# Performance work log

Measured on AMD Instinct MI355X. Metric: run time of the kernel, lower is better.

Reference implementation:

```python
import jax, jax.numpy as jnp
import numpy as np

NUM_GRAPHS = 1024
NODES_PER_GRAPH = 116
DEG = 32
IN_CH = 116
HID = 32
EPS = 1e-5


def setup_inputs() -> dict:
    key = jax.random.key(0)
    ks = jax.random.split(key, 16)
    N = NUM_GRAPHS * NODES_PER_GRAPH
    E = N * DEG
    x = jax.random.normal(ks[0], (N, IN_CH), dtype=jnp.float32)
    # edges stay within each graph: graph id per edge, then random src/dst node in that graph
    gid = jnp.arange(E, dtype=jnp.int64) // (NODES_PER_GRAPH * DEG)
    off = gid * NODES_PER_GRAPH
    src = off + jax.random.randint(ks[1], (E,), 0, NODES_PER_GRAPH, dtype=jnp.int64)
    dst = off + jax.random.randint(ks[2], (E,), 0, NODES_PER_GRAPH, dtype=jnp.int64)
    edge_index = jnp.stack([src, dst], axis=0)
    edge_weight = jax.random.uniform(ks[3], (E,), dtype=jnp.float32)
    batch = jnp.arange(N, dtype=jnp.int64) // NODES_PER_GRAPH
    xavier = lambda k, fi, fo: jax.random.uniform(k, (fi, fo), jnp.float32, -1.0, 1.0) * np.sqrt(6.0 / (fi + fo))
    return {
        "x": x, "edge_index": edge_index, "edge_weight": edge_weight, "batch": batch,
        "W1": xavier(ks[4], IN_CH, HID), "b1": jnp.zeros((HID,), jnp.float32),
        "g1": jnp.ones((HID,), jnp.float32), "be1": jnp.zeros((HID,), jnp.float32),
        "W2": xavier(ks[5], HID, 2 * HID), "b2": jnp.zeros((2 * HID,), jnp.float32),
        "g2": jnp.ones((2 * HID,), jnp.float32), "be2": jnp.zeros((2 * HID,), jnp.float32),
        "Wf1": xavier(ks[6], 4 * HID, HID), "bf1": jnp.zeros((HID,), jnp.float32),
        "gf": jnp.ones((HID,), jnp.float32), "bef": jnp.zeros((HID,), jnp.float32),
        "Wf2": xavier(ks[7], HID, 2), "bf2": jnp.zeros((2,), jnp.float32),
    }


def _gcn_conv(x, row, col, ew, W, b):
    """PyG GCNConv: linear -> add self-loops -> sym-normalized scatter-add -> +bias."""
    N = x.shape[0]
    h = x @ W  # [N, out]
    loop = jnp.arange(N, dtype=row.dtype)
    row_sl = jnp.concatenate([row, loop])
    col_sl = jnp.concatenate([col, loop])
    w_sl = jnp.concatenate([ew, jnp.ones((N,), ew.dtype)])
    deg = jax.ops.segment_sum(w_sl, col_sl, num_segments=N)
    dinv = jnp.where(deg > 0, jax.lax.rsqrt(deg), 0.0)
    norm = dinv[row_sl] * w_sl * dinv[col_sl]  # [E+N]
    msg = h[row_sl] * norm[:, None]            # gather + scale
    out = jax.ops.segment_sum(msg, col_sl, num_segments=N)
    return out + b


def _bn(x, g, b):
    # BatchNorm1d in training mode: biased batch stats over axis 0
    m = jnp.mean(x, axis=0)
    v = jnp.mean(jnp.square(x - m), axis=0)
    return (x - m) * jax.lax.rsqrt(v + EPS) * g + b


def reference(x, edge_index, edge_weight, batch, W1, b1, g1, be1, W2, b2, g2, be2,
              Wf1, bf1, gf, bef, Wf2, bf2):
    row, col = edge_index[0], edge_index[1]
    h = jax.nn.relu(_bn(_gcn_conv(x, row, col, edge_weight, W1, b1), g1, be1))
    h = jax.nn.relu(_bn(_gcn_conv(h, row, col, edge_weight, W2, b2), g2, be2))
    # global mean / max pool over graphs
    counts = jax.ops.segment_sum(jnp.ones((h.shape[0],), h.dtype), batch, num_segments=NUM_GRAPHS)
    x_mean = jax.ops.segment_sum(h, batch, num_segments=NUM_GRAPHS) / counts[:, None]
    x_max = jax.ops.segment_max(h, batch, num_segments=NUM_GRAPHS)
    emb = jnp.concatenate([x_mean, x_max], axis=1)  # [G, 4*HID]
    z = jax.nn.relu(_bn(emb @ Wf1 + bf1, gf, bef))  # dropout = identity (eval)
    return z @ Wf2 + bf2  # [G, num_classes]
```

## Files before the change

### kernel.cpp

```cpp
#include <hip/hip_runtime.h>

#define NPG 116
#define EPG (NPG * 32)
#define HID 32
#define HID2 64
#define EPS 1e-5f

#define WFS 132
#define AS 136
#define YSS 40
#define HPG 7424

using bf16x8 = __attribute__((ext_vector_type(8))) short;
using f32x4  = __attribute__((ext_vector_type(4))) float;

__device__ __forceinline__ unsigned short f2bf(float f) {
  union { float f; unsigned int i; } cv;
  cv.f = f;
  unsigned int x = cv.i;
  x += 0x7fff + ((x >> 16) & 1);
  return (unsigned short)(x >> 16);
}
__device__ __forceinline__ float bf2f(unsigned int u) {
  union { unsigned int i; float f; } cv;
  cv.i = u << 16;
  return cv.f;
}

#define MFMA16(a, b, c) __builtin_amdgcn_mfma_f32_16x16x32_bf16((a), (b), (c), 0, 0, 0)


__global__ __launch_bounds__(256) void k_lin1(const float* __restrict__ x,
                                              const float* __restrict__ W1,
                                              float* __restrict__ h1reg,
                                              int N) {
  __shared__ __align__(16) short W1T[HID * AS];
  const int g = blockIdx.x, tid = threadIdx.x;
  const int nb = g * NPG;
  const int l = tid & 63, w = tid >> 6;
  const int rf = l & 15, kg = l >> 4;

  { int* p = (int*)W1T;
    for (int i = tid; i < HID * AS / 2; i += 256) p[i] = 0; }
  __syncthreads();
  for (int i = tid; i < NPG * HID; i += 256) {
    int k = i >> 5, c = i & 31;
    W1T[c * AS + k] = (short)f2bf(W1[i]);
  }
  __syncthreads();

  unsigned short* lb = (unsigned short*)(h1reg + (size_t)g * 3712);
  for (int t = w; t < 16; t += 4) {
    const int mt = t >> 1, nt = t & 1;
    const int rl = mt * 16 + rf;
    f32x4 acc = {0.f, 0.f, 0.f, 0.f};
#pragma unroll
    for (int kk = 0; kk < 4; ++kk) {
      bf16x8 a;
      if (rl < NPG) {
        const float* xr = x + (size_t)(nb + rl) * NPG;
        if (kk < 3) {
          const float4* xp = (const float4*)(xr + kk * 32 + kg * 8);
          float4 v0 = xp[0], v1 = xp[1];
          a[0] = (short)f2bf(v0.x); a[1] = (short)f2bf(v0.y);
          a[2] = (short)f2bf(v0.z); a[3] = (short)f2bf(v0.w);
          a[4] = (short)f2bf(v1.x); a[5] = (short)f2bf(v1.y);
          a[6] = (short)f2bf(v1.z); a[7] = (short)f2bf(v1.w);
        } else {
          const int k0 = 96 + kg * 8;
#pragma unroll
          for (int j = 0; j < 8; ++j) {
            int k = k0 + j;
            a[j] = (k < NPG) ? (short)f2bf(xr[k]) : (short)0;
          }
        }
      } else {
#pragma unroll
        for (int j = 0; j < 8; ++j) a[j] = 0;
      }
      bf16x8 b = *(const bf16x8*)&W1T[(nt * 16 + rf) * AS + kk * 32 + kg * 8];
      acc = MFMA16(a, b, acc);
    }
    const int col = nt * 16 + rf;
#pragma unroll
    for (int i = 0; i < 4; ++i) {
      int row = mt * 16 + kg * 4 + i;
      if (row < NPG) lb[row * HID + col] = f2bf(acc[i]);
    }
  }
}

__global__ __launch_bounds__(1024) void k_conv1(const int* __restrict__ ei,
                                                const float* __restrict__ ew,
                                                float* __restrict__ h1reg,
                                                float* __restrict__ dinvg,
                                                float* __restrict__ stats,
                                                float* __restrict__ buf,
                                                int N, int E) {
  __shared__ __align__(16) float Wf[NPG * WFS];
  __shared__ __align__(16) short L1T[HID * AS];
  __shared__ float degs[NPG];
  __shared__ float ss[HID], qs[HID];
  const int g = blockIdx.x, tid = threadIdx.x;
  const int nb = g * NPG, e0 = g * EPG;
  const int* rowp = ei;
  const int* colp = ei + E;
  const int l = tid & 63, w = tid >> 6;
  const int rf = l & 15, kg = l >> 4;

  for (int i = tid; i < NPG; i += 1024) degs[i] = 1.0f;
  if (tid < HID) { ss[tid] = 0.0f; qs[tid] = 0.0f; }
  { float4* p = (float4*)Wf;
    for (int i = tid; i < NPG * WFS / 4; i += 1024) p[i] = make_float4(0,0,0,0); }
  { int* p = (int*)L1T;
    for (int i = tid; i < HID * AS / 2; i += 1024) p[i] = 0; }
  __syncthreads();

  for (int e = tid; e < EPG; e += 1024) {
    int eg = e0 + e;
    int s = rowp[eg] - nb, d = colp[eg] - nb;
    float wv = ew[eg];
    atomicAdd(&degs[d], wv);
    atomicAdd(&Wf[d * WFS + s], wv);
  }
  if (tid < NPG) atomicAdd(&Wf[tid * WFS + tid], 1.0f);
  __syncthreads();

  if (tid < NPG) dinvg[nb + tid] = rsqrtf(degs[tid]);
  {
    const unsigned int* lb32 =
        (const unsigned int*)(h1reg + (size_t)g * 3712);
    for (int i = tid; i < NPG * 16; i += 1024) {
      int row = i >> 4, c2 = (i & 15) * 2;
      unsigned int u = lb32[i];
      float dr = rsqrtf(degs[row]);
      L1T[c2 * AS + row] = (short)f2bf(bf2f(u & 0xffffu) * dr);
      L1T[(c2 + 1) * AS + row] = (short)f2bf(bf2f(u >> 16) * dr);
    }
    int* wbg = (int*)(buf + (size_t)g * HPG);
    for (int idx = tid; idx < NPG * 64; idx += 1024) {
      int r = idx >> 6, jj = idx & 63;
      int val = 0;
      if (jj < 58) {
        float2 v = *(const float2*)&Wf[r * WFS + 2 * jj];
        val = (unsigned)f2bf(v.x) | ((unsigned)f2bf(v.y) << 16);
      }
      wbg[idx] = val;
    }
  }
  __syncthreads();

  {
    const int mt = w >> 1, nt = w & 1;
    const int rl = mt * 16 + rf;
    f32x4 acc = {0.f, 0.f, 0.f, 0.f};
#pragma unroll
    for (int kk = 0; kk < 4; ++kk) {
      bf16x8 a;
      if (rl < NPG) {
        const float4* wp = (const float4*)&Wf[rl * WFS + kk * 32 + kg * 8];
        float4 v0 = wp[0], v1 = wp[1];
        a[0] = (short)f2bf(v0.x); a[1] = (short)f2bf(v0.y);
        a[2] = (short)f2bf(v0.z); a[3] = (short)f2bf(v0.w);
        a[4] = (short)f2bf(v1.x); a[5] = (short)f2bf(v1.y);
        a[6] = (short)f2bf(v1.z); a[7] = (short)f2bf(v1.w);
      } else {
#pragma unroll
        for (int j = 0; j < 8; ++j) a[j] = 0;
      }
      bf16x8 b = *(const bf16x8*)&L1T[(nt * 16 + rf) * AS + kk * 32 + kg * 8];
      acc = MFMA16(a, b, acc);
    }
    const int col = nt * 16 + rf;
    float s_ = 0.f, q_ = 0.f;
#pragma unroll
    for (int i = 0; i < 4; ++i) {
      int row = mt * 16 + kg * 4 + i;
      if (row < NPG) {
        float v = rsqrtf(degs[row]) * acc[i];
        h1reg[(size_t)(nb + row) * HID + col] = v;
        s_ += v; q_ += v * v;
      }
    }
    atomicAdd(&ss[col], s_);
    atomicAdd(&qs[col], q_);
  }
  __syncthreads();
  if (tid < HID) {
    atomicAdd(&stats[tid], ss[tid]);
    atomicAdd(&stats[32 + tid], qs[tid]);
  }
}

__global__ __launch_bounds__(1024) void k_conv2(const float* __restrict__ h1,
                                                const float* __restrict__ W2,
                                                const float* __restrict__ g1,
                                                const float* __restrict__ be1,
                                                const float* __restrict__ stats,
                                                const float* __restrict__ dinvg,
                                                float* __restrict__ buf,
                                                float* __restrict__ stats2,
                                                float invN, int N) {
  __shared__ __align__(16) short Ab[128 * AS];
  __shared__ __align__(16) short ysb[128 * YSS];
  __shared__ __align__(16) short W2T[HID2 * YSS];
  __shared__ __align__(16) short L2T[HID2 * AS];
  __shared__ float dv[NPG];
  __shared__ float ss[HID2], qs[HID2];
  __shared__ float a1s[HID], c1s[HID];
  const int g = blockIdx.x, tid = threadIdx.x;
  const int nb = g * NPG;
  const int l = tid & 63, w = tid >> 6;
  const int rf = l & 15, kg = l >> 4;
  float* bufg = buf + (size_t)g * HPG;

  if (tid < HID) {
    float m = stats[tid] * invN;
    float v = stats[32 + tid] * invN - m * m;
    float a = g1[tid] * rsqrtf(v + EPS);
    a1s[tid] = a;
    c1s[tid] = be1[tid] - m * a;
  }
  if (tid < HID2) { ss[tid] = 0.0f; qs[tid] = 0.0f; }
  { int* p = (int*)Ab;
    for (int i = tid; i < 128 * AS / 2; i += 1024) p[i] = 0; }
  { int* p = (int*)L2T;
    for (int i = tid; i < HID2 * AS / 2; i += 1024) p[i] = 0; }
  for (int i = tid; i < HID * HID2; i += 1024) {
    int k = i >> 6, c = i & 63;
    W2T[c * YSS + k] = (short)f2bf(W2[i]);
  }
  for (int i = tid; i < NPG; i += 1024) dv[i] = dinvg[nb + i];
  __syncthreads();

  {
    const float4* hg = (const float4*)(h1 + (size_t)nb * HID);
    for (int i = tid; i < NPG * 8; i += 1024) {
      int r = i >> 3, kc = i & 7, k0 = kc * 4;
      float4 hv = hg[i];
      float dr = dv[r];
      float y0 = dr * fmaxf(0.f, a1s[k0 + 0] * hv.x + c1s[k0 + 0]);
      float y1 = dr * fmaxf(0.f, a1s[k0 + 1] * hv.y + c1s[k0 + 1]);
      float y2 = dr * fmaxf(0.f, a1s[k0 + 2] * hv.z + c1s[k0 + 2]);
      float y3 = dr * fmaxf(0.f, a1s[k0 + 3] * hv.w + c1s[k0 + 3]);
      unsigned int* yp = (unsigned int*)&ysb[r * YSS + k0];
      yp[0] = (unsigned)f2bf(y0) | ((unsigned)f2bf(y1) << 16);
      yp[1] = (unsigned)f2bf(y2) | ((unsigned)f2bf(y3) << 16);
    }
    const int* wbg = (const int*)bufg;
    int* ab = (int*)Ab;
    for (int idx = tid; idx < NPG * 64; idx += 1024) {
      int r = idx >> 6, jj = idx & 63;
      ab[r * (AS / 2) + jj] = wbg[idx];
    }
  }
  __syncthreads();

#pragma unroll
  for (int half = 0; half < 2; ++half) {
    const int t = w + 16 * half;
    const int mt = t >> 2, nt = t & 3;
    bf16x8 a = *(const bf16x8*)&ysb[(mt * 16 + rf) * YSS + kg * 8];
    bf16x8 b = *(const bf16x8*)&W2T[(nt * 16 + rf) * YSS + kg * 8];
    f32x4 acc = {0.f, 0.f, 0.f, 0.f};
    acc = MFMA16(a, b, acc);
    const int col = nt * 16 + rf;
#pragma unroll
    for (int i = 0; i < 4; ++i) {
      int row = mt * 16 + kg * 4 + i;
      if (row < NPG) L2T[col * AS + row] = (short)f2bf(acc[i]);
    }
  }
  __syncthreads();

  {
    const int mt = w >> 1, ntp = (w & 1) * 2;
    f32x4 acc[2] = {{0.f,0.f,0.f,0.f},{0.f,0.f,0.f,0.f}};
#pragma unroll
    for (int kk = 0; kk < 4; ++kk) {
      bf16x8 a = *(const bf16x8*)&Ab[(mt * 16 + rf) * AS + kk * 32 + kg * 8];
#pragma unroll
      for (int u = 0; u < 2; ++u) {
        bf16x8 b = *(const bf16x8*)&L2T[((ntp + u) * 16 + rf) * AS + kk * 32 + kg * 8];
        acc[u] = MFMA16(a, b, acc[u]);
      }
    }
#pragma unroll
    for (int u = 0; u < 2; ++u) {
      const int col = (ntp + u) * 16 + rf;
      float s_ = 0.f, q_ = 0.f;
#pragma unroll
      for (int i = 0; i < 4; ++i) {
        int row = mt * 16 + kg * 4 + i;
        if (row < NPG) {
          float v = dv[row] * acc[u][i];
          bufg[row * HID2 + col] = v;
          s_ += v; q_ += v * v;
        }
      }
      atomicAdd(&ss[col], s_);
      atomicAdd(&qs[col], q_);
    }
  }
  __syncthreads();
  if (tid < HID2) {
    atomicAdd(&stats2[tid], ss[tid]);
    atomicAdd(&stats2[64 + tid], qs[tid]);
  }
}

__global__ __launch_bounds__(256) void k_pool(const float* __restrict__ buf,
                                              const float* __restrict__ g2,
                                              const float* __restrict__ be2,
                                              const float* __restrict__ stats2,
                                              const float* __restrict__ Wf1,
                                              float* __restrict__ z,
                                              float invN, int N) {
  __shared__ float4 psum4[256], pmax4[256];
  __shared__ __align__(16) float emb[128];
  __shared__ __align__(16) float a2s[HID2], c2s[HID2];
  int g = blockIdx.x, tid = threadIdx.x;
  if (tid < HID2) {
    float m = stats2[tid] * invN;
    float v = stats2[64 + tid] * invN - m * m;
    float a = g2[tid] * rsqrtf(v + EPS);
    a2s[tid] = a;
    c2s[tid] = be2[tid] - m * a;
  }
  __syncthreads();
  int c4 = tid & 15, rg = tid >> 4;
  float4 av = ((const float4*)a2s)[c4], bv = ((const float4*)c2s)[c4];
  const float4* h4 = (const float4*)(buf + (size_t)g * HPG);
  float4 s = {0.f, 0.f, 0.f, 0.f};
  float4 mx = {-1e30f, -1e30f, -1e30f, -1e30f};
  for (int n = rg; n < NPG; n += 16) {
    float4 v = h4[n * 16 + c4];
    float4 y;
    y.x = fmaxf(0.f, av.x * v.x + bv.x);
    y.y = fmaxf(0.f, av.y * v.y + bv.y);
    y.z = fmaxf(0.f, av.z * v.z + bv.z);
    y.w = fmaxf(0.f, av.w * v.w + bv.w);
    s.x += y.x; s.y += y.y; s.z += y.z; s.w += y.w;
    mx.x = fmaxf(mx.x, y.x); mx.y = fmaxf(mx.y, y.y);
    mx.z = fmaxf(mx.z, y.z); mx.w = fmaxf(mx.w, y.w);
  }
  psum4[rg * 16 + c4] = s;
  pmax4[rg * 16 + c4] = mx;
  __syncthreads();
  if (tid < 16) {
    float4 S = psum4[tid], M = pmax4[tid];
    for (int j = 1; j < 16; ++j) {
      float4 p = psum4[j * 16 + tid], q = pmax4[j * 16 + tid];
      S.x += p.x; S.y += p.y; S.z += p.z; S.w += p.w;
      M.x = fmaxf(M.x, q.x); M.y = fmaxf(M.y, q.y);
      M.z = fmaxf(M.z, q.z); M.w = fmaxf(M.w, q.w);
    }
    const float inv = 1.0f / NPG;
    ((float4*)emb)[tid] = make_float4(S.x * inv, S.y * inv, S.z * inv, S.w * inv);
    ((float4*)emb)[16 + tid] = M;
  }
  __syncthreads();
  if (tid < 32) {
    float acc = 0.0f;
#pragma unroll
    for (int k = 0; k < 128; ++k) acc += emb[k] * Wf1[k * 32 + tid];
    z[g * 32 + tid] = acc;
  }
}

__global__ __launch_bounds__(256) void k_final(const float* __restrict__ z,
                                               const float* __restrict__ gf,
                                               const float* __restrict__ bef,
                                               const float* __restrict__ Wf2,
                                               const float* __restrict__ bf2,
                                               float* __restrict__ out, int G) {
  __shared__ float ss[32], qs[32], af[32], cf[32];
  __shared__ float w2s[64], b2s[2];
  int tid = threadIdx.x;
  if (tid < 32) { ss[tid] = 0.0f; qs[tid] = 0.0f; }
  if (tid < 64) w2s[tid] = Wf2[tid];
  if (tid < 2) b2s[tid] = bf2[tid];
  __syncthreads();
  const float4* z4 = (const float4*)z;
  int n4 = G * 8;
  float4 s = {0.f, 0.f, 0.f, 0.f}, q = {0.f, 0.f, 0.f, 0.f};
  for (int i = tid; i < n4; i += 256) {
    float4 v = z4[i];
    s.x += v.x; s.y += v.y; s.z += v.z; s.w += v.w;
    q.x += v.x * v.x; q.y += v.y * v.y; q.z += v.z * v.z; q.w += v.w * v.w;
  }
  int cg = (tid & 7) * 4;
  atomicAdd(&ss[cg + 0], s.x); atomicAdd(&ss[cg + 1], s.y);
  atomicAdd(&ss[cg + 2], s.z); atomicAdd(&ss[cg + 3], s.w);
  atomicAdd(&qs[cg + 0], q.x); atomicAdd(&qs[cg + 1], q.y);
  atomicAdd(&qs[cg + 2], q.z); atomicAdd(&qs[cg + 3], q.w);
  __syncthreads();
  if (tid < 32) {
    float invG = 1.0f / G;
    float m = ss[tid] * invG;
    float v = qs[tid] * invG - m * m;
    float a = gf[tid] * rsqrtf(v + EPS);
    af[tid] = a;
    cf[tid] = bef[tid] - m * a;
  }
  __syncthreads();
  for (int g = tid; g < G; g += 256) {
    float o0 = b2s[0], o1 = b2s[1];
    const float4* zr = z4 + g * 8;
#pragma unroll
    for (int kc = 0; kc < 8; ++kc) {
      float4 v = zr[kc];
      int j = 4 * kc;
      float y;
      y = fmaxf(0.f, af[j + 0] * v.x + cf[j + 0]);
      o0 += y * w2s[2 * (j + 0)]; o1 += y * w2s[2 * (j + 0) + 1];
      y = fmaxf(0.f, af[j + 1] * v.y + cf[j + 1]);
      o0 += y * w2s[2 * (j + 1)]; o1 += y * w2s[2 * (j + 1) + 1];
      y = fmaxf(0.f, af[j + 2] * v.z + cf[j + 2]);
      o0 += y * w2s[2 * (j + 2)]; o1 += y * w2s[2 * (j + 2) + 1];
      y = fmaxf(0.f, af[j + 3] * v.w + cf[j + 3]);
      o0 += y * w2s[2 * (j + 3)]; o1 += y * w2s[2 * (j + 3) + 1];
    }
    out[g * 2] = o0;
    out[g * 2 + 1] = o1;
  }
}

extern "C" void kernel_launch(void* const* d_in, const int* in_sizes, int n_in,
                              void* d_out, int out_size, void* d_ws, size_t ws_size,
                              hipStream_t stream) {
  const float* x   = (const float*)d_in[0];
  const int*   ei  = (const int*)d_in[1];
  const float* ew  = (const float*)d_in[2];
  const float* W1  = (const float*)d_in[4];
  const float* g1  = (const float*)d_in[6];
  const float* be1 = (const float*)d_in[7];
  const float* W2  = (const float*)d_in[8];
  const float* g2  = (const float*)d_in[10];
  const float* be2 = (const float*)d_in[11];
  const float* Wf1 = (const float*)d_in[12];
  const float* gf  = (const float*)d_in[14];
  const float* bef = (const float*)d_in[15];
  const float* Wf2 = (const float*)d_in[16];
  const float* bf2 = (const float*)d_in[17];

  int N = in_sizes[3];
  int E = in_sizes[2];
  int G = N / NPG;

  float* ws    = (float*)d_ws;
  float* stats = ws;
  float* dinv  = ws + 256;
  float* h1    = dinv + N;
  float* buf   = h1 + (size_t)N * HID;
  float* z     = buf + (size_t)G * HPG;
  float* out   = (float*)d_out;
  float invN   = 1.0f / (float)N;

  hipMemsetAsync(stats, 0, 256 * sizeof(float), stream);
  k_lin1<<<G, 256, 0, stream>>>(x, W1, h1, N);
  k_conv1<<<G, 1024, 0, stream>>>(ei, ew, h1, dinv, stats, buf, N, E);
  k_conv2<<<G, 1024, 0, stream>>>(h1, W2, g1, be1, stats, dinv, buf,
                                  stats + 64, invN, N);
  k_pool<<<G, 256, 0, stream>>>(buf, g2, be2, stats + 64, Wf1, z, invN, N);
  k_final<<<1, 256, 0, stream>>>(z, gf, bef, Wf2, bf2, out, G);
}
```

Measured before the change: 168.9 us.

## Fuse lin1 into conv1 and build dense adjacency in two row halves

Merges the x@W1 MFMA kernel into the first conv kernel, so h1 stays in registers and shared memory instead of taking a bf16 round trip through global memory, and one launch is removed. The per-graph dense adjacency in LDS is built in two halves of 64 rows, so the block runs with 512 threads and uses less shared memory, which may allow more blocks per CU. In exchange, the edge list is read twice and there are extra barriers and a second zeroing pass.

```diff
diff --git a/kernel.cpp b/kernel.cpp
--- a/kernel.cpp
+++ b/kernel.cpp
@@ -7,6 +7,7 @@
 #define EPS 1e-5f
 
 #define WFS 132
+#define HROWS 64
 #define AS 136
 #define YSS 40
 #define HPG 7424
@@ -21,36 +22,60 @@
   x += 0x7fff + ((x >> 16) & 1);
   return (unsigned short)(x >> 16);
 }
-__device__ __forceinline__ float bf2f(unsigned int u) {
-  union { unsigned int i; float f; } cv;
-  cv.i = u << 16;
-  return cv.f;
-}
 
 #define MFMA16(a, b, c) __builtin_amdgcn_mfma_f32_16x16x32_bf16((a), (b), (c), 0, 0, 0)
 
 
-__global__ __launch_bounds__(256) void k_lin1(const float* __restrict__ x,
-                                              const float* __restrict__ W1,
-                                              float* __restrict__ h1reg,
-                                              int N) {
+__global__ __launch_bounds__(512) void k_conv1(const float* __restrict__ x,
+                                               const int* __restrict__ ei,
+                                               const float* __restrict__ ew,
+                                               const float* __restrict__ W1,
+                                               float* __restrict__ h1,
+                                               float* __restrict__ dinvg,
+                                               float* __restrict__ stats,
+                                               float* __restrict__ buf,
+                                               int N, int E) {
+  __shared__ __align__(16) float Wf[HROWS * WFS];
   __shared__ __align__(16) short W1T[HID * AS];
+  __shared__ __align__(16) short L1T[HID * AS];
+  __shared__ float degs[NPG];
+  __shared__ float ss[HID], qs[HID];
   const int g = blockIdx.x, tid = threadIdx.x;
-  const int nb = g * NPG;
+  const int nb = g * NPG, e0 = g * EPG;
+  const int* rowp = ei;
+  const int* colp = ei + E;
   const int l = tid & 63, w = tid >> 6;
   const int rf = l & 15, kg = l >> 4;
-
-  { int* p = (int*)W1T;
-    for (int i = tid; i < HID * AS / 2; i += 256) p[i] = 0; }
-  __syncthreads();
-  for (int i = tid; i < NPG * HID; i += 256) {
+  int* wbg = (int*)(buf + (size_t)g * HPG);
+
+  for (int i = tid; i < NPG; i += 512) degs[i] = 1.0f;
+  if (tid < HID) { ss[tid] = 0.0f; qs[tid] = 0.0f; }
+  { float4* p = (float4*)Wf;
+    for (int i = tid; i < HROWS * WFS / 4; i += 512) p[i] = make_float4(0,0,0,0); }
+  for (int i = tid; i < HID * 20; i += 512) {
+    int c = i / 20, k = 116 + (i - 20 * (i / 20));
+    W1T[c * AS + k] = 0;
+    L1T[c * AS + k] = 0;
+  }
+  for (int i = tid; i < NPG * HID; i += 512) {
     int k = i >> 5, c = i & 31;
     W1T[c * AS + k] = (short)f2bf(W1[i]);
   }
   __syncthreads();
 
-  unsigned short* lb = (unsigned short*)(h1reg + (size_t)g * 3712);
-  for (int t = w; t < 16; t += 4) {
+  for (int e = tid; e < EPG; e += 512) {
+    int eg = e0 + e;
+    int s = rowp[eg] - nb, d = colp[eg] - nb;
+    float wv = ew[eg];
+    atomicAdd(&degs[d], wv);
+    if (d < HROWS) atomicAdd(&Wf[d * WFS + s], wv);
+  }
+  if (tid < HROWS) atomicAdd(&Wf[tid * WFS + tid], 1.0f);
+
+  f32x4 acc1[2];
+#pragma unroll
+  for (int u = 0; u < 2; ++u) {
+    const int t = w + 8 * u;
     const int mt = t >> 1, nt = t & 1;
     const int rl = mt * 16 + rf;
     f32x4 acc = {0.f, 0.f, 0.f, 0.f};
@@ -81,72 +106,31 @@
       bf16x8 b = *(const bf16x8*)&W1T[(nt * 16 + rf) * AS + kk * 32 + kg * 8];
       acc = MFMA16(a, b, acc);
     }
-    const int col = nt * 16 + rf;
+    acc1[u] = acc;
+  }
+  __syncthreads();
+
+  if (tid < NPG) dinvg[nb + tid] = rsqrtf(degs[tid]);
+#pragma unroll
+  for (int u = 0; u < 2; ++u) {
+    const int t = w + 8 * u;
+    const int mt = t >> 1, nt = t & 1;
 #pragma unroll
     for (int i = 0; i < 4; ++i) {
       int row = mt * 16 + kg * 4 + i;
-      if (row < NPG) lb[row * HID + col] = f2bf(acc[i]);
-    }
-  }
-}
-
-__global__ __launch_bounds__(1024) void k_conv1(const int* __restrict__ ei,
-                                                const float* __restrict__ ew,
-                                                float* __restrict__ h1reg,
-                                                float* __restrict__ dinvg,
-                                                float* __restrict__ stats,
-                                                float* __restrict__ buf,
-                                                int N, int E) {
-  __shared__ __align__(16) float Wf[NPG * WFS];
-  __shared__ __align__(16) short L1T[HID * AS];
-  __shared__ float degs[NPG];
-  __shared__ float ss[HID], qs[HID];
-  const int g = blockIdx.x, tid = threadIdx.x;
-  const int nb = g * NPG, e0 = g * EPG;
-  const int* rowp = ei;
-  const int* colp = ei + E;
-  const int l = tid & 63, w = tid >> 6;
-  const int rf = l & 15, kg = l >> 4;
-
-  for (int i = tid; i < NPG; i += 1024) degs[i] = 1.0f;
-  if (tid < HID) { ss[tid] = 0.0f; qs[tid] = 0.0f; }
-  { float4* p = (float4*)Wf;
-    for (int i = tid; i < NPG * WFS / 4; i += 1024) p[i] = make_float4(0,0,0,0); }
-  { int* p = (int*)L1T;
-    for (int i = tid; i < HID * AS / 2; i += 1024) p[i] = 0; }
-  __syncthreads();
-
-  for (int e = tid; e < EPG; e += 1024) {
-    int eg = e0 + e;
-    int s = rowp[eg] - nb, d = colp[eg] - nb;
-    float wv = ew[eg];
-    atomicAdd(&degs[d], wv);
-    atomicAdd(&Wf[d * WFS + s], wv);
-  }
-  if (tid < NPG) atomicAdd(&Wf[tid * WFS + tid], 1.0f);
-  __syncthreads();
-
-  if (tid < NPG) dinvg[nb + tid] = rsqrtf(degs[tid]);
-  {
-    const unsigned int* lb32 =
-        (const unsigned int*)(h1reg + (size_t)g * 3712);
-    for (int i = tid; i < NPG * 16; i += 1024) {
-      int row = i >> 4, c2 = (i & 15) * 2;
-      unsigned int u = lb32[i];
-      float dr = rsqrtf(degs[row]);
-      L1T[c2 * AS + row] = (short)f2bf(bf2f(u & 0xffffu) * dr);
-      L1T[(c2 + 1) * AS + row] = (short)f2bf(bf2f(u >> 16) * dr);
-    }
-    int* wbg = (int*)(buf + (size_t)g * HPG);
-    for (int idx = tid; idx < NPG * 64; idx += 1024) {
-      int r = idx >> 6, jj = idx & 63;
-      int val = 0;
-      if (jj < 58) {
-        float2 v = *(const float2*)&Wf[r * WFS + 2 * jj];
-        val = (unsigned)f2bf(v.x) | ((unsigned)f2bf(v.y) << 16);
-      }
-      wbg[idx] = val;
-    }
+      if (row < NPG)
+        L1T[(nt * 16 + rf) * AS + row] =
+            (short)f2bf(rsqrtf(degs[row]) * acc1[u][i]);
+    }
+  }
+  for (int idx = tid; idx < HROWS * 64; idx += 512) {
+    int r = idx >> 6, jj = idx & 63;
+    int val = 0;
+    if (jj < 58) {
+      float2 v = *(const float2*)&Wf[r * WFS + 2 * jj];
+      val = (unsigned)f2bf(v.x) | ((unsigned)f2bf(v.y) << 16);
+    }
+    wbg[idx] = val;
   }
   __syncthreads();
 
@@ -156,18 +140,13 @@
     f32x4 acc = {0.f, 0.f, 0.f, 0.f};
 #pragma unroll
     for (int kk = 0; kk < 4; ++kk) {
+      const float4* wp = (const float4*)&Wf[rl * WFS + kk * 32 + kg * 8];
+      float4 v0 = wp[0], v1 = wp[1];
       bf16x8 a;
-      if (rl < NPG) {
-        const float4* wp = (const float4*)&Wf[rl * WFS + kk * 32 + kg * 8];
-        float4 v0 = wp[0], v1 = wp[1];
-        a[0] = (short)f2bf(v0.x); a[1] = (short)f2bf(v0.y);
-        a[2] = (short)f2bf(v0.z); a[3] = (short)f2bf(v0.w);
-        a[4] = (short)f2bf(v1.x); a[5] = (short)f2bf(v1.y);
-        a[6] = (short)f2bf(v1.z); a[7] = (short)f2bf(v1.w);
-      } else {
-#pragma unroll
-        for (int j = 0; j < 8; ++j) a[j] = 0;
-      }
+      a[0] = (short)f2bf(v0.x); a[1] = (short)f2bf(v0.y);
+      a[2] = (short)f2bf(v0.z); a[3] = (short)f2bf(v0.w);
+      a[4] = (short)f2bf(v1.x); a[5] = (short)f2bf(v1.y);
+      a[6] = (short)f2bf(v1.z); a[7] = (short)f2bf(v1.w);
       bf16x8 b = *(const bf16x8*)&L1T[(nt * 16 + rf) * AS + kk * 32 + kg * 8];
       acc = MFMA16(a, b, acc);
     }
@@ -176,9 +155,60 @@
 #pragma unroll
     for (int i = 0; i < 4; ++i) {
       int row = mt * 16 + kg * 4 + i;
-      if (row < NPG) {
-        float v = rsqrtf(degs[row]) * acc[i];
-        h1reg[(size_t)(nb + row) * HID + col] = v;
+      float v = rsqrtf(degs[row]) * acc[i];
+      h1[(size_t)(nb + row) * HID + col] = v;
+      s_ += v; q_ += v * v;
+    }
+    atomicAdd(&ss[col], s_);
+    atomicAdd(&qs[col], q_);
+  }
+  __syncthreads();
+
+  { float4* p = (float4*)Wf;
+    for (int i = tid; i < HROWS * WFS / 4; i += 512) p[i] = make_float4(0,0,0,0); }
+  __syncthreads();
+
+  for (int e = tid; e < EPG; e += 512) {
+    int eg = e0 + e;
+    int s = rowp[eg] - nb, d = colp[eg] - nb;
+    if (d >= HROWS) atomicAdd(&Wf[(d - HROWS) * WFS + s], ew[eg]);
+  }
+  if (tid < NPG - HROWS) atomicAdd(&Wf[tid * WFS + (tid + HROWS)], 1.0f);
+  __syncthreads();
+
+  for (int idx = tid; idx < (NPG - HROWS) * 64; idx += 512) {
+    int r = idx >> 6, jj = idx & 63;
+    int val = 0;
+    if (jj < 58) {
+      float2 v = *(const float2*)&Wf[r * WFS + 2 * jj];
+      val = (unsigned)f2bf(v.x) | ((unsigned)f2bf(v.y) << 16);
+    }
+    wbg[(HROWS + r) * 64 + jj] = val;
+  }
+  {
+    const int mt = w >> 1, nt = w & 1;
+    const int rl = mt * 16 + rf;
+    f32x4 acc = {0.f, 0.f, 0.f, 0.f};
+#pragma unroll
+    for (int kk = 0; kk < 4; ++kk) {
+      const float4* wp = (const float4*)&Wf[rl * WFS + kk * 32 + kg * 8];
+      float4 v0 = wp[0], v1 = wp[1];
+      bf16x8 a;
+      a[0] = (short)f2bf(v0.x); a[1] = (short)f2bf(v0.y);
+      a[2] = (short)f2bf(v0.z); a[3] = (short)f2bf(v0.w);
+      a[4] = (short)f2bf(v1.x); a[5] = (short)f2bf(v1.y);
+      a[6] = (short)f2bf(v1.z); a[7] = (short)f2bf(v1.w);
+      bf16x8 b = *(const bf16x8*)&L1T[(nt * 16 + rf) * AS + kk * 32 + kg * 8];
+      acc = MFMA16(a, b, acc);
+    }
+    const int col = nt * 16 + rf;
+    float s_ = 0.f, q_ = 0.f;
+#pragma unroll
+    for (int i = 0; i < 4; ++i) {
+      int grow = HROWS + mt * 16 + kg * 4 + i;
+      if (grow < NPG) {
+        float v = rsqrtf(degs[grow]) * acc[i];
+        h1[(size_t)(nb + grow) * HID + col] = v;
         s_ += v; q_ += v * v;
       }
     }
@@ -458,8 +488,7 @@
   float invN   = 1.0f / (float)N;
 
   hipMemsetAsync(stats, 0, 256 * sizeof(float), stream);
-  k_lin1<<<G, 256, 0, stream>>>(x, W1, h1, N);
-  k_conv1<<<G, 1024, 0, stream>>>(ei, ew, h1, dinv, stats, buf, N, E);
+  k_conv1<<<G, 512, 0, stream>>>(x, ei, ew, W1, h1, dinv, stats, buf, N, E);
   k_conv2<<<G, 1024, 0, stream>>>(h1, W2, g1, be1, stats, dinv, buf,
                                   stats + 64, invN, N);
   k_pool<<<G, 256, 0, stream>>>(buf, g2, be2, stats + 64, Wf1, z, invN, N);
```

Result: faster. 152.8 us (-9.5%).

## Split adjacency build into own kernel and fuse linear with first aggregation

Applied to the files above, without the earlier changes.

Moves the per-graph dense adjacency construction and degree computation into a separate k_build kernel. The first linear layer and the first aggregation now run in one k_conv1 kernel, so the bf16 h1 staging round trip disappears. Both aggregation kernels read the bf16 adjacency directly from global memory instead of copying it into shared memory first. k_conv2 drops to 512 threads with more MFMA tiles per wave. This cuts shared-memory footprint and copies, but the MFMA A operands now come from global memory loads.

```diff
diff --git a/kernel.cpp b/kernel.cpp
--- a/kernel.cpp
+++ b/kernel.cpp
@@ -6,7 +6,6 @@
 #define HID2 64
 #define EPS 1e-5f
 
-#define WFS 132
 #define AS 136
 #define YSS 40
 #define HPG 7424
@@ -21,39 +20,84 @@
   x += 0x7fff + ((x >> 16) & 1);
   return (unsigned short)(x >> 16);
 }
-__device__ __forceinline__ float bf2f(unsigned int u) {
-  union { unsigned int i; float f; } cv;
-  cv.i = u << 16;
-  return cv.f;
-}
 
 #define MFMA16(a, b, c) __builtin_amdgcn_mfma_f32_16x16x32_bf16((a), (b), (c), 0, 0, 0)
 
 
-__global__ __launch_bounds__(256) void k_lin1(const float* __restrict__ x,
-                                              const float* __restrict__ W1,
-                                              float* __restrict__ h1reg,
-                                              int N) {
+__global__ __launch_bounds__(1024) void k_build(const int* __restrict__ ei,
+                                                const float* __restrict__ ew,
+                                                float* __restrict__ dinvg,
+                                                float* __restrict__ buf,
+                                                int N, int E) {
+  __shared__ float Wf[NPG * NPG];
+  __shared__ float degs[NPG];
+  const int g = blockIdx.x, tid = threadIdx.x;
+  const int nb = g * NPG, e0 = g * EPG;
+  const int* rowp = ei;
+  const int* colp = ei + E;
+
+  for (int i = tid; i < NPG; i += 1024) degs[i] = 1.0f;
+  { float4* p = (float4*)Wf;
+    for (int i = tid; i < NPG * 29; i += 1024) p[i] = make_float4(0,0,0,0); }
+  __syncthreads();
+
+  for (int e = tid; e < EPG; e += 1024) {
+    int eg = e0 + e;
+    int s = rowp[eg] - nb, d = colp[eg] - nb;
+    float wv = ew[eg];
+    atomicAdd(&degs[d], wv);
+    atomicAdd(&Wf[d * NPG + s], wv);
+  }
+  if (tid < NPG) atomicAdd(&Wf[tid * NPG + tid], 1.0f);
+  __syncthreads();
+
+  if (tid < NPG) dinvg[nb + tid] = rsqrtf(degs[tid]);
+  int* wbg = (int*)(buf + (size_t)g * HPG);
+  for (int idx = tid; idx < NPG * 64; idx += 1024) {
+    int r = idx >> 6, jj = idx & 63;
+    int val = 0;
+    if (jj < 58) {
+      float2 v = *(const float2*)&Wf[r * NPG + 2 * jj];
+      val = (unsigned)f2bf(v.x) | ((unsigned)f2bf(v.y) << 16);
+    }
+    wbg[idx] = val;
+  }
+}
+
+__global__ __launch_bounds__(256) void k_conv1(const float* __restrict__ x,
+                                               const float* __restrict__ W1,
+                                               const float* __restrict__ dinvg,
+                                               const float* __restrict__ buf,
+                                               float* __restrict__ h1,
+                                               float* __restrict__ stats,
+                                               int N) {
   __shared__ __align__(16) short W1T[HID * AS];
+  __shared__ __align__(16) short L1T[HID * AS];
+  __shared__ float dv[NPG];
+  __shared__ float ss[HID], qs[HID];
   const int g = blockIdx.x, tid = threadIdx.x;
   const int nb = g * NPG;
   const int l = tid & 63, w = tid >> 6;
   const int rf = l & 15, kg = l >> 4;
 
-  { int* p = (int*)W1T;
-    for (int i = tid; i < HID * AS / 2; i += 256) p[i] = 0; }
-  __syncthreads();
+  if (tid < HID) { ss[tid] = 0.0f; qs[tid] = 0.0f; }
+  for (int i = tid; i < NPG; i += 256) dv[i] = dinvg[nb + i];
+  for (int i = tid; i < HID * 20; i += 256) {
+    int c = i / 20, k = 116 + (i - 20 * (i / 20));
+    W1T[c * AS + k] = 0;
+    L1T[c * AS + k] = 0;
+  }
   for (int i = tid; i < NPG * HID; i += 256) {
     int k = i >> 5, c = i & 31;
     W1T[c * AS + k] = (short)f2bf(W1[i]);
   }
   __syncthreads();
 
-  unsigned short* lb = (unsigned short*)(h1reg + (size_t)g * 3712);
-  for (int t = w; t < 16; t += 4) {
-    const int mt = t >> 1, nt = t & 1;
+#pragma unroll
+  for (int mi = 0; mi < 2; ++mi) {
+    const int mt = w + 4 * mi;
     const int rl = mt * 16 + rf;
-    f32x4 acc = {0.f, 0.f, 0.f, 0.f};
+    f32x4 a0 = {0.f,0.f,0.f,0.f}, a1 = {0.f,0.f,0.f,0.f};
 #pragma unroll
     for (int kk = 0; kk < 4; ++kk) {
       bf16x8 a;
@@ -78,113 +122,61 @@
 #pragma unroll
         for (int j = 0; j < 8; ++j) a[j] = 0;
       }
-      bf16x8 b = *(const bf16x8*)&W1T[(nt * 16 + rf) * AS + kk * 32 + kg * 8];
-      acc = MFMA16(a, b, acc);
-    }
-    const int col = nt * 16 + rf;
+      bf16x8 b0 = *(const bf16x8*)&W1T[rf * AS + kk * 32 + kg * 8];
+      bf16x8 b1 = *(const bf16x8*)&W1T[(16 + rf) * AS + kk * 32 + kg * 8];
+      a0 = MFMA16(a, b0, a0);
+      a1 = MFMA16(a, b1, a1);
+    }
 #pragma unroll
     for (int i = 0; i < 4; ++i) {
       int row = mt * 16 + kg * 4 + i;
-      if (row < NPG) lb[row * HID + col] = f2bf(acc[i]);
-    }
-  }
-}
-
-__global__ __launch_bounds__(1024) void k_conv1(const int* __restrict__ ei,
-                                                const float* __restrict__ ew,
-                                                float* __restrict__ h1reg,
-                                                float* __restrict__ dinvg,
-                                                float* __restrict__ stats,
-                                                float* __restrict__ buf,
-                                                int N, int E) {
-  __shared__ __align__(16) float Wf[NPG * WFS];
-  __shared__ __align__(16) short L1T[HID * AS];
-  __shared__ float degs[NPG];
-  __shared__ float ss[HID], qs[HID];
-  const int g = blockIdx.x, tid = threadIdx.x;
-  const int nb = g * NPG, e0 = g * EPG;
-  const int* rowp = ei;
-  const int* colp = ei + E;
-  const int l = tid & 63, w = tid >> 6;
-  const int rf = l & 15, kg = l >> 4;
-
-  for (int i = tid; i < NPG; i += 1024) degs[i] = 1.0f;
-  if (tid < HID) { ss[tid] = 0.0f; qs[tid] = 0.0f; }
-  { float4* p = (float4*)Wf;
-    for (int i = tid; i < NPG * WFS / 4; i += 1024) p[i] = make_float4(0,0,0,0); }
-  { int* p = (int*)L1T;
-    for (int i = tid; i < HID * AS / 2; i += 1024) p[i] = 0; }
-  __syncthreads();
-
-  for (int e = tid; e < EPG; e += 1024) {
-    int eg = e0 + e;
-    int s = rowp[eg] - nb, d = colp[eg] - nb;
-    float wv = ew[eg];
-    atomicAdd(&degs[d], wv);
-    atomicAdd(&Wf[d * WFS + s], wv);
-  }
-  if (tid < NPG) atomicAdd(&Wf[tid * WFS + tid], 1.0f);
-  __syncthreads();
-
-  if (tid < NPG) dinvg[nb + tid] = rsqrtf(degs[tid]);
-  {
-    const unsigned int* lb32 =
-        (const unsigned int*)(h1reg + (size_t)g * 3712);
-    for (int i = tid; i < NPG * 16; i += 1024) {
-      int row = i >> 4, c2 = (i & 15) * 2;
-      unsigned int u = lb32[i];
-      float dr = rsqrtf(degs[row]);
-      L1T[c2 * AS + row] = (short)f2bf(bf2f(u & 0xffffu) * dr);
-      L1T[(c2 + 1) * AS + row] = (short)f2bf(bf2f(u >> 16) * dr);
-    }
-    int* wbg = (int*)(buf + (size_t)g * HPG);
-    for (int idx = tid; idx < NPG * 64; idx += 1024) {
-      int r = idx >> 6, jj = idx & 63;
-      int val = 0;
-      if (jj < 58) {
-        float2 v = *(const float2*)&Wf[r * WFS + 2 * jj];
-        val = (unsigned)f2bf(v.x) | ((unsigned)f2bf(v.y) << 16);
-      }
-      wbg[idx] = val;
-    }
-  }
-  __syncthreads();
-
-  {
-    const int mt = w >> 1, nt = w & 1;
+      if (row < NPG) {
+        float dr = dv[row];
+        L1T[rf * AS + row] = (short)f2bf(dr * a0[i]);
+        L1T[(16 + rf) * AS + row] = (short)f2bf(dr * a1[i]);
+      }
+    }
+  }
+  __syncthreads();
+
+  const unsigned short* wbs =
+      (const unsigned short*)(buf + (size_t)g * HPG);
+  float s0 = 0.f, q0 = 0.f, s1 = 0.f, q1 = 0.f;
+#pragma unroll
+  for (int mi = 0; mi < 2; ++mi) {
+    const int mt = w + 4 * mi;
     const int rl = mt * 16 + rf;
-    f32x4 acc = {0.f, 0.f, 0.f, 0.f};
+    f32x4 a0 = {0.f,0.f,0.f,0.f}, a1 = {0.f,0.f,0.f,0.f};
 #pragma unroll
     for (int kk = 0; kk < 4; ++kk) {
       bf16x8 a;
       if (rl < NPG) {
-        const float4* wp = (const float4*)&Wf[rl * WFS + kk * 32 + kg * 8];
-        float4 v0 = wp[0], v1 = wp[1];
-        a[0] = (short)f2bf(v0.x); a[1] = (short)f2bf(v0.y);
-        a[2] = (short)f2bf(v0.z); a[3] = (short)f2bf(v0.w);
-        a[4] = (short)f2bf(v1.x); a[5] = (short)f2bf(v1.y);
-        a[6] = (short)f2bf(v1.z); a[7] = (short)f2bf(v1.w);
+        a = *(const bf16x8*)&wbs[rl * 128 + kk * 32 + kg * 8];
       } else {
 #pragma unroll
         for (int j = 0; j < 8; ++j) a[j] = 0;
       }
-      bf16x8 b = *(const bf16x8*)&L1T[(nt * 16 + rf) * AS + kk * 32 + kg * 8];
-      acc = MFMA16(a, b, acc);
-    }
-    const int col = nt * 16 + rf;
-    float s_ = 0.f, q_ = 0.f;
+      bf16x8 b0 = *(const bf16x8*)&L1T[rf * AS + kk * 32 + kg * 8];
+      bf16x8 b1 = *(const bf16x8*)&L1T[(16 + rf) * AS + kk * 32 + kg * 8];
+      a0 = MFMA16(a, b0, a0);
+      a1 = MFMA16(a, b1, a1);
+    }
 #pragma unroll
     for (int i = 0; i < 4; ++i) {
       int row = mt * 16 + kg * 4 + i;
       if (row < NPG) {
-        float v = rsqrtf(degs[row]) * acc[i];
-        h1reg[(size_t)(nb + row) * HID + col] = v;
-        s_ += v; q_ += v * v;
-      }
-    }
-    atomicAdd(&ss[col], s_);
-    atomicAdd(&qs[col], q_);
-  }
+        float dr = dv[row];
+        float v0 = dr * a0[i], v1 = dr * a1[i];
+        float* hrow = h1 + (size_t)(nb + row) * HID;
+        hrow[rf] = v0;
+        hrow[16 + rf] = v1;
+        s0 += v0; q0 += v0 * v0;
+        s1 += v1; q1 += v1 * v1;
+      }
+    }
+  }
+  atomicAdd(&ss[rf], s0);      atomicAdd(&qs[rf], q0);
+  atomicAdd(&ss[16 + rf], s1); atomicAdd(&qs[16 + rf], q1);
   __syncthreads();
   if (tid < HID) {
     atomicAdd(&stats[tid], ss[tid]);
@@ -192,16 +184,15 @@
   }
 }
 
-__global__ __launch_bounds__(1024) void k_conv2(const float* __restrict__ h1,
-                                                const float* __restrict__ W2,
-                                                const float* __restrict__ g1,
-                                                const float* __restrict__ be1,
-                                                const float* __restrict__ stats,
-                                                const float* __restrict__ dinvg,
-                                                float* __restrict__ buf,
-                                                float* __restrict__ stats2,
-                                                float invN, int N) {
-  __shared__ __align__(16) short Ab[128 * AS];
+__global__ __launch_bounds__(512) void k_conv2(const float* __restrict__ h1,
+                                               const float* __restrict__ W2,
+                                               const float* __restrict__ g1,
+                                               const float* __restrict__ be1,
+                                               const float* __restrict__ stats,
+                                               const float* __restrict__ dinvg,
+                                               float* __restrict__ buf,
+                                               float* __restrict__ stats2,
+                                               float invN, int N) {
   __shared__ __align__(16) short ysb[128 * YSS];
   __shared__ __align__(16) short W2T[HID2 * YSS];
   __shared__ __align__(16) short L2T[HID2 * AS];
@@ -222,20 +213,20 @@
     c1s[tid] = be1[tid] - m * a;
   }
   if (tid < HID2) { ss[tid] = 0.0f; qs[tid] = 0.0f; }
-  { int* p = (int*)Ab;
-    for (int i = tid; i < 128 * AS / 2; i += 1024) p[i] = 0; }
+  { int* p = (int*)ysb;
+    for (int i = tid; i < 128 * YSS / 2; i += 512) p[i] = 0; }
   { int* p = (int*)L2T;
-    for (int i = tid; i < HID2 * AS / 2; i += 1024) p[i] = 0; }
-  for (int i = tid; i < HID * HID2; i += 1024) {
+    for (int i = tid; i < HID2 * AS / 2; i += 512) p[i] = 0; }
+  for (int i = tid; i < HID * HID2; i += 512) {
     int k = i >> 6, c = i & 63;
     W2T[c * YSS + k] = (short)f2bf(W2[i]);
   }
-  for (int i = tid; i < NPG; i += 1024) dv[i] = dinvg[nb + i];
+  for (int i = tid; i < NPG; i += 512) dv[i] = dinvg[nb + i];
   __syncthreads();
 
   {
     const float4* hg = (const float4*)(h1 + (size_t)nb * HID);
-    for (int i = tid; i < NPG * 8; i += 1024) {
+    for (int i = tid; i < NPG * 8; i += 512) {
       int r = i >> 3, kc = i & 7, k0 = kc * 4;
       float4 hv = hg[i];
       float dr = dv[r];
@@ -247,18 +238,12 @@
       yp[0] = (unsigned)f2bf(y0) | ((unsigned)f2bf(y1) << 16);
       yp[1] = (unsigned)f2bf(y2) | ((unsigned)f2bf(y3) << 16);
     }
-    const int* wbg = (const int*)bufg;
-    int* ab = (int*)Ab;
-    for (int idx = tid; idx < NPG * 64; idx += 1024) {
-      int r = idx >> 6, jj = idx & 63;
-      ab[r * (AS / 2) + jj] = wbg[idx];
-    }
-  }
-  __syncthreads();
-
-#pragma unroll
-  for (int half = 0; half < 2; ++half) {
-    const int t = w + 16 * half;
+  }
+  __syncthreads();
+
+#pragma unroll
+  for (int u = 0; u < 4; ++u) {
+    const int t = w + 8 * u;
     const int mt = t >> 2, nt = t & 3;
     bf16x8 a = *(const bf16x8*)&ysb[(mt * 16 + rf) * YSS + kg * 8];
     bf16x8 b = *(const bf16x8*)&W2T[(nt * 16 + rf) * YSS + kg * 8];
@@ -274,26 +259,36 @@
   __syncthreads();
 
   {
-    const int mt = w >> 1, ntp = (w & 1) * 2;
-    f32x4 acc[2] = {{0.f,0.f,0.f,0.f},{0.f,0.f,0.f,0.f}};
+    const unsigned short* wbs = (const unsigned short*)bufg;
+    const int mt = w;
+    const int rl = mt * 16 + rf;
+    f32x4 acc[4];
+#pragma unroll
+    for (int nt = 0; nt < 4; ++nt) acc[nt] = (f32x4){0.f, 0.f, 0.f, 0.f};
 #pragma unroll
     for (int kk = 0; kk < 4; ++kk) {
-      bf16x8 a = *(const bf16x8*)&Ab[(mt * 16 + rf) * AS + kk * 32 + kg * 8];
-#pragma unroll
-      for (int u = 0; u < 2; ++u) {
-        bf16x8 b = *(const bf16x8*)&L2T[((ntp + u) * 16 + rf) * AS + kk * 32 + kg * 8];
-        acc[u] = MFMA16(a, b, acc[u]);
-      }
-    }
-#pragma unroll
-    for (int u = 0; u < 2; ++u) {
-      const int col = (ntp + u) * 16 + rf;
+      bf16x8 a;
+      if (rl < NPG) {
+        a = *(const bf16x8*)&wbs[rl * 128 + kk * 32 + kg * 8];
+      } else {
+#pragma unroll
+        for (int j = 0; j < 8; ++j) a[j] = 0;
+      }
+#pragma unroll
+      for (int nt = 0; nt < 4; ++nt) {
+        bf16x8 b = *(const bf16x8*)&L2T[(nt * 16 + rf) * AS + kk * 32 + kg * 8];
+        acc[nt] = MFMA16(a, b, acc[nt]);
+      }
+    }
+#pragma unroll
+    for (int nt = 0; nt < 4; ++nt) {
+      const int col = nt * 16 + rf;
       float s_ = 0.f, q_ = 0.f;
 #pragma unroll
       for (int i = 0; i < 4; ++i) {
         int row = mt * 16 + kg * 4 + i;
         if (row < NPG) {
-          float v = dv[row] * acc[u][i];
+          float v = dv[row] * acc[nt][i];
           bufg[row * HID2 + col] = v;
           s_ += v; q_ += v * v;
         }
@@ -458,10 +453,10 @@
   float invN   = 1.0f / (float)N;
 
   hipMemsetAsync(stats, 0, 256 * sizeof(float), stream);
-  k_lin1<<<G, 256, 0, stream>>>(x, W1, h1, N);
-  k_conv1<<<G, 1024, 0, stream>>>(ei, ew, h1, dinv, stats, buf, N, E);
-  k_conv2<<<G, 1024, 0, stream>>>(h1, W2, g1, be1, stats, dinv, buf,
-                                  stats + 64, invN, N);
+  k_build<<<G, 1024, 0, stream>>>(ei, ew, dinv, buf, N, E);
+  k_conv1<<<G, 256, 0, stream>>>(x, W1, dinv, buf, h1, stats, N);
+  k_conv2<<<G, 512, 0, stream>>>(h1, W2, g1, be1, stats, dinv, buf,
+                                 stats + 64, invN, N);
   k_pool<<<G, 256, 0, stream>>>(buf, g2, be2, stats + 64, Wf1, z, invN, N);
   k_final<<<1, 256, 0, stream>>>(z, gf, bef, Wf2, bf2, out, G);
 }
```

Result: slower. 173.7 us (+2.9%).
